# Kernel tuning notes

Hardware: AMD Instinct MI355X
Metric: run time of the kernel (lower is better)

The kernel has to match this reference:

```python
import jax, jax.numpy as jnp
import numpy as np

NUM_QRYS = 300
NUM_CLASSES = 80
NUM_PAIRS = 4_000_000
NMS_CANDIDATES = 1000
NMS_THR = 0.65
MAX_SEGS = 100
REFINED_WEIGHT = 2.0
FH = FW = 256  # final mask grid resolution


def setup_inputs() -> dict:
    key = jax.random.key(0)
    k1, k2, k3, k4, k5, k6, k7 = jax.random.split(key, 7)
    cls_logits = jax.random.normal(k1, (NUM_QRYS, NUM_CLASSES + 1), jnp.float32)
    # valid xyxy boxes in normalized [0,1] coords
    b = jax.random.uniform(k2, (NUM_QRYS, 4), jnp.float32)
    x1 = b[:, 0] * 0.7
    y1 = b[:, 1] * 0.7
    x2 = x1 + 0.05 + b[:, 2] * 0.25
    y2 = y1 + 0.05 + b[:, 3] * 0.25
    pred_boxes = jnp.stack([x1, y1, x2, y2], axis=1)
    seg_logits = jax.random.normal(k3, (NUM_PAIRS,), jnp.float32)
    key_xy = jax.random.uniform(k4, (NUM_PAIRS, 2), jnp.float32)
    qry_ids = jax.random.randint(k5, (NUM_PAIRS,), 0, NUM_QRYS, jnp.int32)
    refined_mask = jax.random.randint(k6, (NUM_PAIRS,), 0, 2, jnp.int32).astype(bool)
    map_ids = jax.random.randint(k7, (NUM_PAIRS,), 0, 4, jnp.int32)
    return {"cls_logits": cls_logits, "pred_boxes": pred_boxes, "seg_logits": seg_logits,
            "key_xy": key_xy, "qry_ids": qry_ids, "refined_mask": refined_mask, "map_ids": map_ids}


def _box_iou(boxes):  # boxes: [C,4] xyxy -> [C,C]
    x1 = jnp.maximum(boxes[:, None, 0], boxes[None, :, 0])
    y1 = jnp.maximum(boxes[:, None, 1], boxes[None, :, 1])
    x2 = jnp.minimum(boxes[:, None, 2], boxes[None, :, 2])
    y2 = jnp.minimum(boxes[:, None, 3], boxes[None, :, 3])
    inter = jnp.clip(x2 - x1, 0.0) * jnp.clip(y2 - y1, 0.0)
    area = (boxes[:, 2] - boxes[:, 0]) * (boxes[:, 3] - boxes[:, 1])
    union = area[:, None] + area[None, :] - inter
    return inter / jnp.maximum(union, 1e-9)


def _nms_keep(iou, thr):
    # greedy NMS over score-sorted candidates (rows already in descending score order)
    C = iou.shape[0]
    idx = jnp.arange(C)
    def body(i, keep):
        sup = (iou[i] > thr) & (idx > i) & keep[i]
        return keep & ~sup
    return jax.lax.fori_loop(0, C, body, jnp.ones(C, dtype=bool))


def reference(cls_logits, pred_boxes, seg_logits, key_xy, qry_ids, refined_mask, map_ids):
    num_qrys = cls_logits.shape[0]
    # expand per-query class scores -> flat predictions (batch_size = 1)
    scores = jax.nn.sigmoid(cls_logits[:, :-1]).reshape(-1)          # [Q*C]
    feat_ids = jnp.repeat(jnp.arange(num_qrys), NUM_CLASSES)          # [Q*C]
    labels = jnp.tile(jnp.arange(NUM_CLASSES), num_qrys)              # [Q*C]
    # top-k candidates before NMS
    top_scores, cand = jax.lax.top_k(scores, NMS_CANDIDATES)
    cand_feats = feat_ids[cand]
    cand_labels = labels[cand]
    # class-aware (batched) NMS: offset boxes per label so classes don't suppress each other
    offs = cand_labels.astype(pred_boxes.dtype)[:, None] * 4.0
    cand_boxes = pred_boxes[cand_feats] + offs
    keep = _nms_keep(_box_iou(cand_boxes), NMS_THR)
    kept_scores = jnp.where(keep, top_scores, -jnp.inf)
    sel_scores, sel = jax.lax.top_k(kept_scores, MAX_SEGS)
    sel_scores = jnp.where(jnp.isfinite(sel_scores), sel_scores, 0.0)
    sel_feats = cand_feats[sel]
    # assemble per-query mask logit maps from sparse query-key pairs (scatter-max)
    px = jnp.clip((key_xy[:, 0] * FW).astype(jnp.int32), 0, FW - 1)
    py = jnp.clip((key_xy[:, 1] * FH).astype(jnp.int32), 0, FH - 1)
    w_logits = jnp.where(refined_mask, REFINED_WEIGHT * seg_logits, seg_logits)
    flat = qry_ids * (FH * FW) + py * FW + px                          # [num_pairs]
    qry_maps = jnp.full((num_qrys * FH * FW,), -1e4, cls_logits.dtype).at[flat].max(w_logits)
    qry_maps = qry_maps.reshape(num_qrys, FH, FW)
    mask_probs = jax.nn.sigmoid(qry_maps[sel_feats])                   # [MAX_SEGS, FH, FW]
    # score-weighted soft masks (float output; thresholding at mask_thr yields bool masks)
    return sel_scores[:, None, None] * mask_probs
```

## Files before the change

kernel.cpp:

```cpp
#include <hip/hip_runtime.h>

#define NQ        300
#define NC        80
#define NE        24000
#define CAND      1000
#define KSEL      100
#define NPAIRS    4000000
#define HB        4096
#define FHW       65536
#define NMS_THR_F 0.65f
#define MAPS_INIT 0x39E3BFFFu

__device__ __forceinline__ unsigned enc_f32(float f) {
    unsigned u = __float_as_uint(f);
    return (u & 0x80000000u) ? ~u : (u | 0x80000000u);
}
__device__ __forceinline__ float dec_f32(unsigned k) {
    unsigned u = (k & 0x80000000u) ? (k ^ 0x80000000u) : ~k;
    return __uint_as_float(u);
}

__global__ void k_init_maps(uint4* __restrict__ maps) {
    int i = blockIdx.x * 256 + threadIdx.x;
    uint4 v; v.x = v.y = v.z = v.w = MAPS_INIT;
    maps[i] = v;
}

__global__ __launch_bounds__(1024) void k_select_sort(
    const float* __restrict__ cls,
    const float* __restrict__ pboxes,
    float4* __restrict__ cboxes, float* __restrict__ cscore,
    int* __restrict__ cfeat, int* __restrict__ clabel)
{
    __shared__ unsigned long long sbuf[4096];
    unsigned* hist = (unsigned*)sbuf;
    __shared__ unsigned subhist[64];
    __shared__ int sB, sT, sAbove, sCount, sN;
    int tid = threadIdx.x;

    for (int b = tid; b < HB; b += 1024) hist[b] = 0u;
    if (tid < 64) subhist[tid] = 0u;
    __syncthreads();

    unsigned long long lk[24];
    #pragma unroll
    for (int k = 0; k < 24; k++) {
        int e = tid + (k << 10);
        if (e < NE) {
            int q = e / NC, c = e - q * NC;
            float x = cls[q * (NC + 1) + c];
            float s = 1.f / (1.f + expf(-x));
            unsigned bits = __float_as_uint(s);
            lk[k] = ((unsigned long long)bits << 32) | (unsigned)(0xFFFFFFFFu - (unsigned)e);
            atomicAdd(&hist[bits >> 18], 1u);
        }
    }
    __syncthreads();

    if (tid == 0) {
        int acc = 0, B = 0;
        for (int b = HB - 1; b >= 0; b--) {
            acc += (int)hist[b];
            if (acc >= CAND) { B = b; break; }
        }
        sB = B; sAbove = acc - (int)hist[B]; sCount = 0;
    }
    __syncthreads();
    unsigned B = (unsigned)sB;

    #pragma unroll
    for (int k = 0; k < 24; k++) {
        int e = tid + (k << 10);
        if (e < NE && (unsigned)(lk[k] >> 50) == B)
            atomicAdd(&subhist[(unsigned)(lk[k] >> 44) & 63u], 1u);
    }
    __syncthreads();
    if (tid == 0) {
        int acc2 = sAbove, T = 0;
        for (int t = 63; t >= 0; t--) {
            acc2 += (int)subhist[t];
            if (acc2 >= CAND) { T = t; break; }
        }
        sT = T; sN = acc2;
    }
    __syncthreads();
    unsigned T = (unsigned)sT;

    #pragma unroll
    for (int k = 0; k < 24; k++) {
        int e = tid + (k << 10);
        if (e < NE) {
            unsigned long long key = lk[k];
            unsigned bkt = (unsigned)(key >> 50);
            unsigned sub = (unsigned)(key >> 44) & 63u;
            if (bkt > B || (bkt == B && sub >= T)) {
                int pos = atomicAdd(&sCount, 1);
                if (pos < 4096) sbuf[pos] = key;
            }
        }
    }
    __syncthreads();
    int n = min(sN, 4096);

    if (n <= 1024) {
        unsigned long long r = (tid < n) ? sbuf[tid] : 0ULL;
        for (int k = 2; k <= 1024; k <<= 1) {
            for (int j = k >> 1; j > 0; j >>= 1) {
                unsigned long long p;
                if (j >= 64) {
                    sbuf[tid] = r; __syncthreads();
                    p = sbuf[tid ^ j]; __syncthreads();
                } else {
                    p = __shfl_xor(r, j, 64);
                }
                bool d = (tid & k) != 0, lower = (tid & j) == 0;
                r = (d != lower) ? (r > p ? r : p) : (r < p ? r : p);
            }
        }
        sbuf[tid] = r;
        __syncthreads();
    } else {
        int nsort = 2048; while (nsort < n) nsort <<= 1;
        for (int i = n + tid; i < nsort; i += 1024) sbuf[i] = 0ULL;
        __syncthreads();
        for (int k = 2; k <= nsort; k <<= 1) {
            for (int j = k >> 1; j > 0; j >>= 1) {
                for (int i = tid; i < nsort; i += 1024) {
                    int ixj = i ^ j;
                    if (ixj > i) {
                        unsigned long long a = sbuf[i], b = sbuf[ixj];
                        bool up = ((i & k) == 0);
                        if (up ? (a < b) : (a > b)) { sbuf[i] = b; sbuf[ixj] = a; }
                    }
                }
                __syncthreads();
            }
        }
    }

    if (tid < CAND) {
        unsigned long long key = sbuf[tid];
        unsigned bits = (unsigned)(key >> 32);
        unsigned e = 0xFFFFFFFFu - (unsigned)(key & 0xFFFFFFFFu);
        int feat = (int)e / NC, lab = (int)e - feat * NC;
        cscore[tid] = __uint_as_float(bits);
        cfeat[tid]  = feat;
        clabel[tid] = lab;
        float off = 4.f * (float)lab;
        float4 b;
        b.x = pboxes[feat * 4 + 0] + off; b.y = pboxes[feat * 4 + 1] + off;
        b.z = pboxes[feat * 4 + 2] + off; b.w = pboxes[feat * 4 + 3] + off;
        cboxes[tid] = b;
    }
}

__global__ __launch_bounds__(64) void k_nms(
    const float4* __restrict__ cboxes, const int* __restrict__ clabel,
    int* __restrict__ keepflag)
{
    int lab = blockIdx.x, lane = threadIdx.x;
    __shared__ int list[256];
    int base = 0;
    for (int c = 0; c < CAND; c += 64) {
        int i = c + lane;
        bool m = (i < CAND) && (clabel[i] == lab);
        unsigned long long bal = __ballot(m);
        int rank = __popcll(bal & ((1ULL << lane) - 1ULL));
        if (m && base + rank < 256) list[base + rank] = i;
        base += __popcll(bal);
    }
    __syncthreads();
    int n = min(base, 256);

    float4 bx[4]; float area[4];
    unsigned keepm = 0;
    #pragma unroll
    for (int s = 0; s < 4; s++) {
        int j = (s << 6) + lane;
        if (j < n) {
            bx[s] = cboxes[list[j]];
            area[s] = (bx[s].z - bx[s].x) * (bx[s].w - bx[s].y);
            keepm |= (1u << s);
        }
    }
    #pragma unroll
    for (int slot = 0; slot < 4; slot++) {
        int i0 = slot << 6;
        if (i0 >= n) break;
        int iend = min(64, n - i0);
        for (int l = 0; l < iend; l++) {
            int i = i0 + l;
            unsigned km = __shfl(keepm, l);
            bool keep_i = (km >> slot) & 1u;
            float bix = __shfl(bx[slot].x, l), biy = __shfl(bx[slot].y, l);
            float biz = __shfl(bx[slot].z, l), biw = __shfl(bx[slot].w, l);
            float ai  = __shfl(area[slot], l);
            if (keep_i) {
                #pragma unroll
                for (int s2 = 0; s2 < 4; s2++) {
                    int j = (s2 << 6) + lane;
                    if (j > i && j < n && ((keepm >> s2) & 1u)) {
                        float xx1 = fmaxf(bix, bx[s2].x), yy1 = fmaxf(biy, bx[s2].y);
                        float xx2 = fminf(biz, bx[s2].z), yy2 = fminf(biw, bx[s2].w);
                        float inter = fmaxf(xx2 - xx1, 0.f) * fmaxf(yy2 - yy1, 0.f);
                        float uni = ai + area[s2] - inter;
                        if (inter / fmaxf(uni, 1e-9f) > NMS_THR_F) keepm &= ~(1u << s2);
                    }
                }
            }
        }
    }
    #pragma unroll
    for (int s = 0; s < 4; s++) {
        int j = (s << 6) + lane;
        if (j < n) keepflag[list[j]] = (keepm >> s) & 1u;
    }
}

__global__ __launch_bounds__(64) void k_pick(
    const float* __restrict__ cscore, const int* __restrict__ cfeat,
    const int* __restrict__ keepflag,
    float* __restrict__ sel_score, int* __restrict__ sel_slot,
    int* __restrict__ qry2slot,
    const unsigned* __restrict__ refined_raw, unsigned* __restrict__ mode_flag)
{
    int lane = threadIdx.x;
    __shared__ float ss[KSEL];
    __shared__ int   sf[KSEL];
    __shared__ int   q2s[NQ];

    unsigned any = 0;
    for (int i = lane; i < 4096; i += 64) if (refined_raw[i] > 1u) any = 1;
    unsigned mode = (__ballot(any != 0) != 0ULL) ? 1u : 0u;

    int base = 0;
    for (int c = 0; c < CAND; c += 64) {
        int i = c + lane;
        bool k = (i < CAND) && (keepflag[i] != 0);
        unsigned long long bal = __ballot(k);
        int rank = __popcll(bal & ((1ULL << lane) - 1ULL));
        int pos = base + rank;
        if (k && pos < KSEL) { ss[pos] = cscore[i]; sf[pos] = cfeat[i]; }
        base += __popcll(bal);
    }
    for (int q = lane; q < NQ; q += 64) q2s[q] = -1;
    __syncthreads();
    if (lane == 0) {
        int nsel = min(base, KSEL), nslots = 0;
        for (int s = 0; s < KSEL; s++) {
            if (s < nsel) {
                int f = sf[s];
                int sl = q2s[f];
                if (sl < 0) { sl = nslots++; q2s[f] = sl; }
                sel_slot[s] = sl; sel_score[s] = ss[s];
            } else {
                sel_slot[s] = -1; sel_score[s] = 0.f;
            }
        }
        *mode_flag = mode;
    }
    __syncthreads();
    for (int q = lane; q < NQ; q += 64) qry2slot[q] = q2s[q];
}

__global__ __launch_bounds__(256) void k_scatter(
    const float* __restrict__ seg, const float2* __restrict__ xy,
    const int* __restrict__ qry, const unsigned* __restrict__ refined_raw,
    const int* __restrict__ qry2slot, const unsigned* __restrict__ mode_flag,
    unsigned* __restrict__ maps)
{
    int t = blockIdx.x * 256 + threadIdx.x;
    int base = t << 2;
    if (base >= NPAIRS) return;

    int4 q4 = ((const int4*)qry)[t];
    int s0 = qry2slot[q4.x], s1 = qry2slot[q4.y];
    int s2 = qry2slot[q4.z], s3 = qry2slot[q4.w];
    if ((s0 & s1 & s2 & s3) < 0) return;

    float4 sg   = ((const float4*)seg)[t];
    float4 xy01 = ((const float4*)xy)[2 * t];
    float4 xy23 = ((const float4*)xy)[2 * t + 1];
    unsigned r0, r1, r2, r3;
    if (*mode_flag) {
        unsigned rb = refined_raw[t];
        r0 = rb & 255u; r1 = (rb >> 8) & 255u; r2 = (rb >> 16) & 255u; r3 = rb >> 24;
    } else {
        uint4 rr = ((const uint4*)refined_raw)[t];
        r0 = rr.x; r1 = rr.y; r2 = rr.z; r3 = rr.w;
    }

    #define DO_PAIR(S, PX, PY, W, R)                                              \
        if (S >= 0) {                                                             \
            int px = min(max((int)((PX) * 256.f), 0), 255);                       \
            int py = min(max((int)((PY) * 256.f), 0), 255);                       \
            float w = (R) ? 2.f * (W) : (W);                                      \
            atomicMax(&maps[S * FHW + py * 256 + px], enc_f32(w));                \
        }
    DO_PAIR(s0, xy01.x, xy01.y, sg.x, r0)
    DO_PAIR(s1, xy01.z, xy01.w, sg.y, r1)
    DO_PAIR(s2, xy23.x, xy23.y, sg.z, r2)
    DO_PAIR(s3, xy23.z, xy23.w, sg.w, r3)
    #undef DO_PAIR
}

__global__ __launch_bounds__(256) void k_output(
    const uint4* __restrict__ maps4,
    const float* __restrict__ sel_score, const int* __restrict__ sel_slot,
    float4* __restrict__ out4)
{
    int i = blockIdx.x * 256 + threadIdx.x;
    int s = i >> 14;
    float sc = sel_score[s];
    int slot = sel_slot[s];
    float4 v = {0.f, 0.f, 0.f, 0.f};
    if (slot >= 0) {
        uint4 m = maps4[slot * (FHW / 4) + (i & 16383)];
        v.x = sc / (1.f + expf(-dec_f32(m.x)));
        v.y = sc / (1.f + expf(-dec_f32(m.y)));
        v.z = sc / (1.f + expf(-dec_f32(m.z)));
        v.w = sc / (1.f + expf(-dec_f32(m.w)));
    }
    out4[i] = v;
}

extern "C" void kernel_launch(void* const* d_in, const int* in_sizes, int n_in,
                              void* d_out, int out_size, void* d_ws, size_t ws_size,
                              hipStream_t stream) {
    const float*    cls     = (const float*)d_in[0];
    const float*    pboxes  = (const float*)d_in[1];
    const float*    seg     = (const float*)d_in[2];
    const float2*   xy      = (const float2*)d_in[3];
    const int*      qry     = (const int*)d_in[4];
    const unsigned* refined = (const unsigned*)d_in[5];
    float* out = (float*)d_out;

    char* ws = (char*)d_ws;
    unsigned*  maps      = (unsigned*)ws;
    float4*    cboxes    = (float4*)(ws + 26214400);
    float*     cscore    = (float*) (ws + 26230400);
    int*       cfeat     = (int*)   (ws + 26234400);
    int*       clabel    = (int*)   (ws + 26238400);
    int*       keepflag  = (int*)   (ws + 26242400);
    float*     sel_score = (float*) (ws + 26246400);
    int*       sel_slot  = (int*)   (ws + 26246800);
    int*       qry2slot  = (int*)   (ws + 26247200);
    unsigned*  mode_flag = (unsigned*)(ws + 26248400);

    k_init_maps  <<<6400, 256, 0, stream>>>((uint4*)maps);
    k_select_sort<<<1, 1024, 0, stream>>>(cls, pboxes, cboxes, cscore, cfeat, clabel);
    k_nms        <<<NC, 64, 0, stream>>>(cboxes, clabel, keepflag);
    k_pick       <<<1, 64, 0, stream>>>(cscore, cfeat, keepflag, sel_score, sel_slot,
                                        qry2slot, refined, mode_flag);
    k_scatter    <<<3907, 256, 0, stream>>>(seg, xy, qry, refined, qry2slot, mode_flag, maps);
    k_output     <<<6400, 256, 0, stream>>>((const uint4*)maps, sel_score, sel_slot,
                                            (float4*)out);
}
```

Baseline: 256.0 us.

## Fuse map init into select, merge NMS and pick, widen scatter to 8 pairs

Map initialization now runs in extra blocks of the top-k selection kernel. Per-class NMS and final selection are merged into one 1024-thread block, with 16 waves each taking classes in turn and keep flags held in shared memory. The scatter kernel now handles 8 pairs per thread and stages the query-to-slot table in shared memory, issuing all loads before the barrier. Together these cut two launches and their inter-kernel gaps, at the cost of running NMS on a single workgroup instead of 80.

```diff
diff --git a/kernel.cpp b/kernel.cpp
--- a/kernel.cpp
+++ b/kernel.cpp
@@ -20,23 +20,25 @@
     return __uint_as_float(u);
 }
 
-__global__ void k_init_maps(uint4* __restrict__ maps) {
-    int i = blockIdx.x * 256 + threadIdx.x;
-    uint4 v; v.x = v.y = v.z = v.w = MAPS_INIT;
-    maps[i] = v;
-}
-
-__global__ __launch_bounds__(1024) void k_select_sort(
+__global__ __launch_bounds__(1024) void k_init_select(
     const float* __restrict__ cls,
     const float* __restrict__ pboxes,
     float4* __restrict__ cboxes, float* __restrict__ cscore,
-    int* __restrict__ cfeat, int* __restrict__ clabel)
+    int* __restrict__ cfeat, int* __restrict__ clabel,
+    uint4* __restrict__ maps)
 {
     __shared__ unsigned long long sbuf[4096];
     unsigned* hist = (unsigned*)sbuf;
     __shared__ unsigned subhist[64];
     __shared__ int sB, sT, sAbove, sCount, sN;
     int tid = threadIdx.x;
+
+    if (blockIdx.x != 0) {
+        int i = (blockIdx.x - 1) * 1024 + tid;
+        uint4 v; v.x = v.y = v.z = v.w = MAPS_INIT;
+        maps[i] = v;
+        return;
+    }
 
     for (int b = tid; b < HB; b += 1024) hist[b] = 0u;
     if (tid < 64) subhist[tid] = 0u;
@@ -154,99 +156,109 @@
     }
 }
 
-__global__ __launch_bounds__(64) void k_nms(
+__global__ __launch_bounds__(1024) void k_nms_pick(
     const float4* __restrict__ cboxes, const int* __restrict__ clabel,
-    int* __restrict__ keepflag)
-{
-    int lab = blockIdx.x, lane = threadIdx.x;
-    __shared__ int list[256];
-    int base = 0;
-    for (int c = 0; c < CAND; c += 64) {
-        int i = c + lane;
-        bool m = (i < CAND) && (clabel[i] == lab);
-        unsigned long long bal = __ballot(m);
-        int rank = __popcll(bal & ((1ULL << lane) - 1ULL));
-        if (m && base + rank < 256) list[base + rank] = i;
-        base += __popcll(bal);
-    }
-    __syncthreads();
-    int n = min(base, 256);
-
-    float4 bx[4]; float area[4];
-    unsigned keepm = 0;
-    #pragma unroll
-    for (int s = 0; s < 4; s++) {
-        int j = (s << 6) + lane;
-        if (j < n) {
-            bx[s] = cboxes[list[j]];
-            area[s] = (bx[s].z - bx[s].x) * (bx[s].w - bx[s].y);
-            keepm |= (1u << s);
-        }
-    }
-    #pragma unroll
-    for (int slot = 0; slot < 4; slot++) {
-        int i0 = slot << 6;
-        if (i0 >= n) break;
-        int iend = min(64, n - i0);
-        for (int l = 0; l < iend; l++) {
-            int i = i0 + l;
-            unsigned km = __shfl(keepm, l);
-            bool keep_i = (km >> slot) & 1u;
-            float bix = __shfl(bx[slot].x, l), biy = __shfl(bx[slot].y, l);
-            float biz = __shfl(bx[slot].z, l), biw = __shfl(bx[slot].w, l);
-            float ai  = __shfl(area[slot], l);
-            if (keep_i) {
-                #pragma unroll
-                for (int s2 = 0; s2 < 4; s2++) {
-                    int j = (s2 << 6) + lane;
-                    if (j > i && j < n && ((keepm >> s2) & 1u)) {
-                        float xx1 = fmaxf(bix, bx[s2].x), yy1 = fmaxf(biy, bx[s2].y);
-                        float xx2 = fminf(biz, bx[s2].z), yy2 = fminf(biw, bx[s2].w);
-                        float inter = fmaxf(xx2 - xx1, 0.f) * fmaxf(yy2 - yy1, 0.f);
-                        float uni = ai + area[s2] - inter;
-                        if (inter / fmaxf(uni, 1e-9f) > NMS_THR_F) keepm &= ~(1u << s2);
-                    }
-                }
-            }
-        }
-    }
-    #pragma unroll
-    for (int s = 0; s < 4; s++) {
-        int j = (s << 6) + lane;
-        if (j < n) keepflag[list[j]] = (keepm >> s) & 1u;
-    }
-}
-
-__global__ __launch_bounds__(64) void k_pick(
     const float* __restrict__ cscore, const int* __restrict__ cfeat,
-    const int* __restrict__ keepflag,
     float* __restrict__ sel_score, int* __restrict__ sel_slot,
     int* __restrict__ qry2slot,
     const unsigned* __restrict__ refined_raw, unsigned* __restrict__ mode_flag)
 {
-    int lane = threadIdx.x;
+    __shared__ int list[16][256];
+    __shared__ int keepf[CAND];
     __shared__ float ss[KSEL];
     __shared__ int   sf[KSEL];
     __shared__ int   q2s[NQ];
-
-    unsigned any = 0;
-    for (int i = lane; i < 4096; i += 64) if (refined_raw[i] > 1u) any = 1;
-    unsigned mode = (__ballot(any != 0) != 0ULL) ? 1u : 0u;
-
-    int base = 0;
-    for (int c = 0; c < CAND; c += 64) {
-        int i = c + lane;
-        bool k = (i < CAND) && (keepflag[i] != 0);
-        unsigned long long bal = __ballot(k);
-        int rank = __popcll(bal & ((1ULL << lane) - 1ULL));
-        int pos = base + rank;
-        if (k && pos < KSEL) { ss[pos] = cscore[i]; sf[pos] = cfeat[i]; }
-        base += __popcll(bal);
-    }
-    for (int q = lane; q < NQ; q += 64) q2s[q] = -1;
-    __syncthreads();
-    if (lane == 0) {
-        int nsel = min(base, KSEL), nslots = 0;
+    __shared__ unsigned smode;
+    __shared__ int sbase;
+
+    int tid  = threadIdx.x;
+    int wave = tid >> 6, lane = tid & 63;
+    int* mylist = list[wave];
+
+    for (int i = tid; i < CAND; i += 1024) keepf[i] = 0;
+    for (int q = tid; q < NQ; q += 1024) q2s[q] = -1;
+    __syncthreads();
+
+    for (int lab = wave; lab < NC; lab += 16) {
+        int base = 0;
+        for (int c = 0; c < CAND; c += 64) {
+            int i = c + lane;
+            bool m = (i < CAND) && (clabel[i] == lab);
+            unsigned long long bal = __ballot(m);
+            int rank = __popcll(bal & ((1ULL << lane) - 1ULL));
+            if (m && base + rank < 256) mylist[base + rank] = i;
+            base += __popcll(bal);
+        }
+        int n = min(base, 256);
+
+        float4 bx[4]; float area[4];
+        unsigned keepm = 0;
+        #pragma unroll
+        for (int s = 0; s < 4; s++) {
+            int j = (s << 6) + lane;
+            if (j < n) {
+                bx[s] = cboxes[mylist[j]];
+                area[s] = (bx[s].z - bx[s].x) * (bx[s].w - bx[s].y);
+                keepm |= (1u << s);
+            }
+        }
+        #pragma unroll
+        for (int slot = 0; slot < 4; slot++) {
+            int i0 = slot << 6;
+            if (i0 >= n) break;
+            int iend = min(64, n - i0);
+            for (int l = 0; l < iend; l++) {
+                int i = i0 + l;
+                unsigned km = __shfl(keepm, l);
+                bool keep_i = (km >> slot) & 1u;
+                float bix = __shfl(bx[slot].x, l), biy = __shfl(bx[slot].y, l);
+                float biz = __shfl(bx[slot].z, l), biw = __shfl(bx[slot].w, l);
+                float ai  = __shfl(area[slot], l);
+                if (keep_i) {
+                    #pragma unroll
+                    for (int s2 = 0; s2 < 4; s2++) {
+                        int j = (s2 << 6) + lane;
+                        if (j > i && j < n && ((keepm >> s2) & 1u)) {
+                            float xx1 = fmaxf(bix, bx[s2].x), yy1 = fmaxf(biy, bx[s2].y);
+                            float xx2 = fminf(biz, bx[s2].z), yy2 = fminf(biw, bx[s2].w);
+                            float inter = fmaxf(xx2 - xx1, 0.f) * fmaxf(yy2 - yy1, 0.f);
+                            float uni = ai + area[s2] - inter;
+                            if (inter / fmaxf(uni, 1e-9f) > NMS_THR_F) keepm &= ~(1u << s2);
+                        }
+                    }
+                }
+            }
+        }
+        #pragma unroll
+        for (int s = 0; s < 4; s++) {
+            int j = (s << 6) + lane;
+            if (j < n) keepf[mylist[j]] = (keepm >> s) & 1u;
+        }
+    }
+    __syncthreads();
+
+    if (wave == 0) {
+        unsigned any = 0;
+        for (int i = lane; i < 4096; i += 64) if (refined_raw[i] > 1u) any = 1;
+        unsigned mode = (__ballot(any != 0) != 0ULL) ? 1u : 0u;
+        if (lane == 0) smode = mode;
+
+        int base = 0;
+        for (int c = 0; c < CAND; c += 64) {
+            int i = c + lane;
+            bool k = (i < CAND) && (keepf[i] != 0);
+            unsigned long long bal = __ballot(k);
+            int rank = __popcll(bal & ((1ULL << lane) - 1ULL));
+            int pos = base + rank;
+            if (k && pos < KSEL) { ss[pos] = cscore[i]; sf[pos] = cfeat[i]; }
+            base += __popcll(bal);
+        }
+        if (lane == 0) sbase = base;
+    }
+    __syncthreads();
+
+    if (tid == 0) {
+        int nsel = min(sbase, KSEL), nslots = 0;
         for (int s = 0; s < KSEL; s++) {
             if (s < nsel) {
                 int f = sf[s];
@@ -257,38 +269,53 @@
                 sel_slot[s] = -1; sel_score[s] = 0.f;
             }
         }
-        *mode_flag = mode;
-    }
-    __syncthreads();
-    for (int q = lane; q < NQ; q += 64) qry2slot[q] = q2s[q];
+        *mode_flag = smode;
+    }
+    __syncthreads();
+    for (int q = tid; q < NQ; q += 1024) qry2slot[q] = q2s[q];
 }
 
 __global__ __launch_bounds__(256) void k_scatter(
-    const float* __restrict__ seg, const float2* __restrict__ xy,
-    const int* __restrict__ qry, const unsigned* __restrict__ refined_raw,
+    const float4* __restrict__ seg4, const float4* __restrict__ xy4,
+    const int4* __restrict__ qry4, const unsigned* __restrict__ refined_raw,
     const int* __restrict__ qry2slot, const unsigned* __restrict__ mode_flag,
     unsigned* __restrict__ maps)
 {
-    int t = blockIdx.x * 256 + threadIdx.x;
-    int base = t << 2;
-    if (base >= NPAIRS) return;
-
-    int4 q4 = ((const int4*)qry)[t];
-    int s0 = qry2slot[q4.x], s1 = qry2slot[q4.y];
-    int s2 = qry2slot[q4.z], s3 = qry2slot[q4.w];
-    if ((s0 & s1 & s2 & s3) < 0) return;
-
-    float4 sg   = ((const float4*)seg)[t];
-    float4 xy01 = ((const float4*)xy)[2 * t];
-    float4 xy23 = ((const float4*)xy)[2 * t + 1];
-    unsigned r0, r1, r2, r3;
-    if (*mode_flag) {
-        unsigned rb = refined_raw[t];
-        r0 = rb & 255u; r1 = (rb >> 8) & 255u; r2 = (rb >> 16) & 255u; r3 = rb >> 24;
-    } else {
-        uint4 rr = ((const uint4*)refined_raw)[t];
-        r0 = rr.x; r1 = rr.y; r2 = rr.z; r3 = rr.w;
-    }
+    __shared__ int q2s[NQ];
+    int tid = threadIdx.x;
+    int t = blockIdx.x * 256 + tid;
+    bool act = (t < (NPAIRS / 8));
+
+    int4 qa = {0,0,0,0}, qb = {0,0,0,0};
+    float4 sa = {0,0,0,0}, sb = {0,0,0,0};
+    float4 x0 = {0,0,0,0}, x1 = {0,0,0,0}, x2 = {0,0,0,0}, x3 = {0,0,0,0};
+    unsigned r0=0,r1=0,r2=0,r3=0,r4=0,r5=0,r6=0,r7=0;
+
+    if (act) {
+        qa = qry4[2*t];     qb = qry4[2*t+1];
+        sa = seg4[2*t];     sb = seg4[2*t+1];
+        x0 = xy4[4*t];      x1 = xy4[4*t+1];
+        x2 = xy4[4*t+2];    x3 = xy4[4*t+3];
+        unsigned mode = *mode_flag;
+        if (mode) {
+            unsigned rw0 = refined_raw[2*t], rw1 = refined_raw[2*t+1];
+            r0 = rw0 & 255u; r1 = (rw0 >> 8) & 255u; r2 = (rw0 >> 16) & 255u; r3 = rw0 >> 24;
+            r4 = rw1 & 255u; r5 = (rw1 >> 8) & 255u; r6 = (rw1 >> 16) & 255u; r7 = rw1 >> 24;
+        } else {
+            uint4 rr0 = ((const uint4*)refined_raw)[2*t];
+            uint4 rr1 = ((const uint4*)refined_raw)[2*t+1];
+            r0 = rr0.x; r1 = rr0.y; r2 = rr0.z; r3 = rr0.w;
+            r4 = rr1.x; r5 = rr1.y; r6 = rr1.z; r7 = rr1.w;
+        }
+    }
+
+    for (int q = tid; q < NQ; q += 256) q2s[q] = qry2slot[q];
+    __syncthreads();
+    if (!act) return;
+
+    int s0 = q2s[qa.x], s1 = q2s[qa.y], s2 = q2s[qa.z], s3 = q2s[qa.w];
+    int s4 = q2s[qb.x], s5 = q2s[qb.y], s6 = q2s[qb.z], s7 = q2s[qb.w];
+    if ((s0 & s1 & s2 & s3 & s4 & s5 & s6 & s7) < 0) return;
 
     #define DO_PAIR(S, PX, PY, W, R)                                              \
         if (S >= 0) {                                                             \
@@ -297,10 +324,14 @@
             float w = (R) ? 2.f * (W) : (W);                                      \
             atomicMax(&maps[S * FHW + py * 256 + px], enc_f32(w));                \
         }
-    DO_PAIR(s0, xy01.x, xy01.y, sg.x, r0)
-    DO_PAIR(s1, xy01.z, xy01.w, sg.y, r1)
-    DO_PAIR(s2, xy23.x, xy23.y, sg.z, r2)
-    DO_PAIR(s3, xy23.z, xy23.w, sg.w, r3)
+    DO_PAIR(s0, x0.x, x0.y, sa.x, r0)
+    DO_PAIR(s1, x0.z, x0.w, sa.y, r1)
+    DO_PAIR(s2, x1.x, x1.y, sa.z, r2)
+    DO_PAIR(s3, x1.z, x1.w, sa.w, r3)
+    DO_PAIR(s4, x2.x, x2.y, sb.x, r4)
+    DO_PAIR(s5, x2.z, x2.w, sb.y, r5)
+    DO_PAIR(s6, x3.x, x3.y, sb.z, r6)
+    DO_PAIR(s7, x3.z, x3.w, sb.w, r7)
     #undef DO_PAIR
 }
 
@@ -329,9 +360,9 @@
                               hipStream_t stream) {
     const float*    cls     = (const float*)d_in[0];
     const float*    pboxes  = (const float*)d_in[1];
-    const float*    seg     = (const float*)d_in[2];
-    const float2*   xy      = (const float2*)d_in[3];
-    const int*      qry     = (const int*)d_in[4];
+    const float4*   seg4    = (const float4*)d_in[2];
+    const float4*   xy4     = (const float4*)d_in[3];
+    const int4*     qry4    = (const int4*)d_in[4];
     const unsigned* refined = (const unsigned*)d_in[5];
     float* out = (float*)d_out;
 
@@ -341,18 +372,17 @@
     float*     cscore    = (float*) (ws + 26230400);
     int*       cfeat     = (int*)   (ws + 26234400);
     int*       clabel    = (int*)   (ws + 26238400);
-    int*       keepflag  = (int*)   (ws + 26242400);
     float*     sel_score = (float*) (ws + 26246400);
     int*       sel_slot  = (int*)   (ws + 26246800);
     int*       qry2slot  = (int*)   (ws + 26247200);
     unsigned*  mode_flag = (unsigned*)(ws + 26248400);
 
-    k_init_maps  <<<6400, 256, 0, stream>>>((uint4*)maps);
-    k_select_sort<<<1, 1024, 0, stream>>>(cls, pboxes, cboxes, cscore, cfeat, clabel);
-    k_nms        <<<NC, 64, 0, stream>>>(cboxes, clabel, keepflag);
-    k_pick       <<<1, 64, 0, stream>>>(cscore, cfeat, keepflag, sel_score, sel_slot,
-                                        qry2slot, refined, mode_flag);
-    k_scatter    <<<3907, 256, 0, stream>>>(seg, xy, qry, refined, qry2slot, mode_flag, maps);
+    k_init_select<<<1601, 1024, 0, stream>>>(cls, pboxes, cboxes, cscore, cfeat, clabel,
+                                             (uint4*)maps);
+    k_nms_pick   <<<1, 1024, 0, stream>>>(cboxes, clabel, cscore, cfeat,
+                                          sel_score, sel_slot, qry2slot, refined, mode_flag);
+    k_scatter    <<<1954, 256, 0, stream>>>(seg4, xy4, qry4, refined, qry2slot, mode_flag,
+                                            (unsigned*)maps);
     k_output     <<<6400, 256, 0, stream>>>((const uint4*)maps, sel_score, sel_slot,
                                             (float4*)out);
 }
```

New measurement: 260.7 us. About the same (+1.8%).

## Bin selected pairs per slot, then build mask tiles in shared memory

Applied to the files above, without the earlier changes.

Replaces the global atomicMax scatter into a 26 MB per-slot map, and the kernel that initialised it, with a two-phase scheme. A staging kernel buckets the selected pairs into per-slot bins using block-local histograms and one global tail counter per slot. A tile kernel then rebuilds each 8192-pixel tile with shared-memory atomicMax and writes the sigmoid-weighted output directly. This removes the map initialisation pass and the global-memory atomics. The cost is that each tile block rescans the whole bin of its slot, so every bin is read eight times. A fixed per-slot capacity of 32768 records silently drops overflow pairs when a query has more pairs than that.

```diff
diff --git a/kernel.cpp b/kernel.cpp
--- a/kernel.cpp
+++ b/kernel.cpp
@@ -11,6 +11,9 @@
 #define NMS_THR_F 0.65f
 #define MAPS_INIT 0x39E3BFFFu
 
+#define NBLK_A    977
+#define SLOT_CAP  32768
+
 __device__ __forceinline__ unsigned enc_f32(float f) {
     unsigned u = __float_as_uint(f);
     return (u & 0x80000000u) ? ~u : (u | 0x80000000u);
@@ -20,23 +23,20 @@
     return __uint_as_float(u);
 }
 
-__global__ void k_init_maps(uint4* __restrict__ maps) {
-    int i = blockIdx.x * 256 + threadIdx.x;
-    uint4 v; v.x = v.y = v.z = v.w = MAPS_INIT;
-    maps[i] = v;
-}
-
-__global__ __launch_bounds__(1024) void k_select_sort(
+__global__ __launch_bounds__(1024) void k_select(
     const float* __restrict__ cls,
     const float* __restrict__ pboxes,
     float4* __restrict__ cboxes, float* __restrict__ cscore,
-    int* __restrict__ cfeat, int* __restrict__ clabel)
+    int* __restrict__ cfeat, int* __restrict__ clabel,
+    unsigned* __restrict__ slot_tail)
 {
     __shared__ unsigned long long sbuf[4096];
     unsigned* hist = (unsigned*)sbuf;
     __shared__ unsigned subhist[64];
     __shared__ int sB, sT, sAbove, sCount, sN;
     int tid = threadIdx.x;
+
+    if (tid < KSEL) slot_tail[tid] = 0u;
 
     for (int b = tid; b < HB; b += 1024) hist[b] = 0u;
     if (tid < 64) subhist[tid] = 0u;
@@ -263,65 +263,112 @@
     for (int q = lane; q < NQ; q += 64) qry2slot[q] = q2s[q];
 }
 
-__global__ __launch_bounds__(256) void k_scatter(
-    const float* __restrict__ seg, const float2* __restrict__ xy,
-    const int* __restrict__ qry, const unsigned* __restrict__ refined_raw,
+__global__ __launch_bounds__(1024) void k_stage(
+    const float4* __restrict__ seg4, const float4* __restrict__ xy4,
+    const int4* __restrict__ qry4, const unsigned* __restrict__ refined_raw,
     const int* __restrict__ qry2slot, const unsigned* __restrict__ mode_flag,
-    unsigned* __restrict__ maps)
+    unsigned long long* __restrict__ bins, unsigned* __restrict__ slot_tail)
 {
-    int t = blockIdx.x * 256 + threadIdx.x;
-    int base = t << 2;
-    if (base >= NPAIRS) return;
-
-    int4 q4 = ((const int4*)qry)[t];
-    int s0 = qry2slot[q4.x], s1 = qry2slot[q4.y];
-    int s2 = qry2slot[q4.z], s3 = qry2slot[q4.w];
-    if ((s0 & s1 & s2 & s3) < 0) return;
-
-    float4 sg   = ((const float4*)seg)[t];
-    float4 xy01 = ((const float4*)xy)[2 * t];
-    float4 xy23 = ((const float4*)xy)[2 * t + 1];
-    unsigned r0, r1, r2, r3;
-    if (*mode_flag) {
-        unsigned rb = refined_raw[t];
-        r0 = rb & 255u; r1 = (rb >> 8) & 255u; r2 = (rb >> 16) & 255u; r3 = rb >> 24;
-    } else {
-        uint4 rr = ((const uint4*)refined_raw)[t];
-        r0 = rr.x; r1 = rr.y; r2 = rr.z; r3 = rr.w;
-    }
-
-    #define DO_PAIR(S, PX, PY, W, R)                                              \
-        if (S >= 0) {                                                             \
-            int px = min(max((int)((PX) * 256.f), 0), 255);                       \
-            int py = min(max((int)((PY) * 256.f), 0), 255);                       \
-            float w = (R) ? 2.f * (W) : (W);                                      \
-            atomicMax(&maps[S * FHW + py * 256 + px], enc_f32(w));                \
-        }
-    DO_PAIR(s0, xy01.x, xy01.y, sg.x, r0)
-    DO_PAIR(s1, xy01.z, xy01.w, sg.y, r1)
-    DO_PAIR(s2, xy23.x, xy23.y, sg.z, r2)
-    DO_PAIR(s3, xy23.z, xy23.w, sg.w, r3)
-    #undef DO_PAIR
-}
-
-__global__ __launch_bounds__(256) void k_output(
-    const uint4* __restrict__ maps4,
+    __shared__ unsigned hist[KSEL];
+    __shared__ unsigned gbase[KSEL];
+    int tid = threadIdx.x, b = blockIdx.x;
+    if (tid < KSEL) hist[tid] = 0u;
+    __syncthreads();
+
+    int t = b * 1024 + tid;
+    unsigned addr[4], encw[4], rnk[4]; int nloc = 0;
+    if (t < (NPAIRS / 4)) {
+        int4 q = qry4[t];
+        int s0 = qry2slot[q.x], s1 = qry2slot[q.y];
+        int s2 = qry2slot[q.z], s3 = qry2slot[q.w];
+        if ((s0 & s1 & s2 & s3) >= 0 || s0 >= 0 || s1 >= 0 || s2 >= 0 || s3 >= 0) {
+            float4 sg   = seg4[t];
+            float4 xy01 = xy4[2 * t], xy23 = xy4[2 * t + 1];
+            unsigned r0, r1, r2, r3;
+            if (*mode_flag) {
+                unsigned rb = refined_raw[t];
+                r0 = rb & 255u; r1 = (rb >> 8) & 255u; r2 = (rb >> 16) & 255u; r3 = rb >> 24;
+            } else {
+                uint4 rr = ((const uint4*)refined_raw)[t];
+                r0 = rr.x; r1 = rr.y; r2 = rr.z; r3 = rr.w;
+            }
+            #define MK_REC(S, PX, PY, W, R)                                       \
+                if (S >= 0) {                                                     \
+                    int px = min(max((int)((PX) * 256.f), 0), 255);               \
+                    int py = min(max((int)((PY) * 256.f), 0), 255);               \
+                    float w = (R) ? 2.f * (W) : (W);                              \
+                    addr[nloc] = ((unsigned)S << 16) | ((unsigned)py << 8) | (unsigned)px; \
+                    encw[nloc] = enc_f32(w);                                      \
+                    rnk[nloc]  = atomicAdd(&hist[S], 1u);                         \
+                    nloc++;                                                       \
+                }
+            MK_REC(s0, xy01.x, xy01.y, sg.x, r0)
+            MK_REC(s1, xy01.z, xy01.w, sg.y, r1)
+            MK_REC(s2, xy23.x, xy23.y, sg.z, r2)
+            MK_REC(s3, xy23.z, xy23.w, sg.w, r3)
+            #undef MK_REC
+        }
+    }
+    __syncthreads();
+    if (tid < KSEL && hist[tid] > 0u)
+        gbase[tid] = atomicAdd(&slot_tail[tid], hist[tid]);
+    __syncthreads();
+
+    for (int k = 0; k < nloc; k++) {
+        unsigned s = addr[k] >> 16;
+        unsigned pos = gbase[s] + rnk[k];
+        if (pos < SLOT_CAP)
+            bins[(size_t)s * SLOT_CAP + pos] =
+                ((unsigned long long)encw[k] << 32) | addr[k];
+    }
+}
+
+__global__ __launch_bounds__(1024) void k_tile_out(
+    const unsigned long long* __restrict__ bins,
+    const unsigned* __restrict__ slot_tail,
     const float* __restrict__ sel_score, const int* __restrict__ sel_slot,
     float4* __restrict__ out4)
 {
-    int i = blockIdx.x * 256 + threadIdx.x;
-    int s = i >> 14;
-    float sc = sel_score[s];
-    int slot = sel_slot[s];
-    float4 v = {0.f, 0.f, 0.f, 0.f};
-    if (slot >= 0) {
-        uint4 m = maps4[slot * (FHW / 4) + (i & 16383)];
-        v.x = sc / (1.f + expf(-dec_f32(m.x)));
-        v.y = sc / (1.f + expf(-dec_f32(m.y)));
-        v.z = sc / (1.f + expf(-dec_f32(m.z)));
-        v.w = sc / (1.f + expf(-dec_f32(m.w)));
-    }
-    out4[i] = v;
+    __shared__ unsigned tile[8192];
+    int tid = threadIdx.x;
+    int i = blockIdx.x >> 3, h = blockIdx.x & 7;
+    int slot = sel_slot[i];
+    float sc = sel_score[i];
+    long obase = (long)i * (FHW / 4) + h * 2048;
+
+    if (slot < 0) {
+        float4 z = {0.f, 0.f, 0.f, 0.f};
+        out4[obase + tid] = z;
+        out4[obase + 1024 + tid] = z;
+        return;
+    }
+
+    #pragma unroll
+    for (int k = 0; k < 8; k++) tile[tid + (k << 10)] = MAPS_INIT;
+    __syncthreads();
+
+    unsigned tot = min(slot_tail[slot], (unsigned)SLOT_CAP);
+    const unsigned long long* seg = bins + (size_t)slot * SLOT_CAP;
+    for (unsigned j = tid; j < tot; j += 1024) {
+        unsigned long long r = seg[j];
+        unsigned addr = (unsigned)r;
+        if (((addr >> 13) & 7u) == (unsigned)h)
+            atomicMax(&tile[addr & 8191u], (unsigned)(r >> 32));
+    }
+    __syncthreads();
+
+    #pragma unroll
+    for (int k = 0; k < 2; k++) {
+        int j = tid + (k << 10);
+        unsigned m0 = tile[4 * j + 0], m1 = tile[4 * j + 1];
+        unsigned m2 = tile[4 * j + 2], m3 = tile[4 * j + 3];
+        float4 v;
+        v.x = sc / (1.f + expf(-dec_f32(m0)));
+        v.y = sc / (1.f + expf(-dec_f32(m1)));
+        v.z = sc / (1.f + expf(-dec_f32(m2)));
+        v.w = sc / (1.f + expf(-dec_f32(m3)));
+        out4[obase + j] = v;
+    }
 }
 
 extern "C" void kernel_launch(void* const* d_in, const int* in_sizes, int n_in,
@@ -329,30 +376,32 @@
                               hipStream_t stream) {
     const float*    cls     = (const float*)d_in[0];
     const float*    pboxes  = (const float*)d_in[1];
-    const float*    seg     = (const float*)d_in[2];
-    const float2*   xy      = (const float2*)d_in[3];
-    const int*      qry     = (const int*)d_in[4];
+    const float4*   seg4    = (const float4*)d_in[2];
+    const float4*   xy4     = (const float4*)d_in[3];
+    const int4*     qry4    = (const int4*)d_in[4];
     const unsigned* refined = (const unsigned*)d_in[5];
     float* out = (float*)d_out;
 
     char* ws = (char*)d_ws;
-    unsigned*  maps      = (unsigned*)ws;
-    float4*    cboxes    = (float4*)(ws + 26214400);
-    float*     cscore    = (float*) (ws + 26230400);
-    int*       cfeat     = (int*)   (ws + 26234400);
-    int*       clabel    = (int*)   (ws + 26238400);
-    int*       keepflag  = (int*)   (ws + 26242400);
-    float*     sel_score = (float*) (ws + 26246400);
-    int*       sel_slot  = (int*)   (ws + 26246800);
-    int*       qry2slot  = (int*)   (ws + 26247200);
-    unsigned*  mode_flag = (unsigned*)(ws + 26248400);
-
-    k_init_maps  <<<6400, 256, 0, stream>>>((uint4*)maps);
-    k_select_sort<<<1, 1024, 0, stream>>>(cls, pboxes, cboxes, cscore, cfeat, clabel);
-    k_nms        <<<NC, 64, 0, stream>>>(cboxes, clabel, keepflag);
-    k_pick       <<<1, 64, 0, stream>>>(cscore, cfeat, keepflag, sel_score, sel_slot,
-                                        qry2slot, refined, mode_flag);
-    k_scatter    <<<3907, 256, 0, stream>>>(seg, xy, qry, refined, qry2slot, mode_flag, maps);
-    k_output     <<<6400, 256, 0, stream>>>((const uint4*)maps, sel_score, sel_slot,
-                                            (float4*)out);
-}
+    unsigned long long* bins = (unsigned long long*)ws;
+    unsigned*  slot_tail = (unsigned*)(ws + 26214400);
+    float4*    cboxes    = (float4*)  (ws + 26214800);
+    float*     cscore    = (float*)   (ws + 26230800);
+    int*       cfeat     = (int*)     (ws + 26234800);
+    int*       clabel    = (int*)     (ws + 26238800);
+    int*       keepflag  = (int*)     (ws + 26242800);
+    float*     sel_score = (float*)   (ws + 26246800);
+    int*       sel_slot  = (int*)     (ws + 26247200);
+    int*       qry2slot  = (int*)     (ws + 26247600);
+    unsigned*  mode_flag = (unsigned*)(ws + 26248800);
+
+    k_select  <<<1, 1024, 0, stream>>>(cls, pboxes, cboxes, cscore, cfeat, clabel,
+                                       slot_tail);
+    k_nms     <<<NC, 64, 0, stream>>>(cboxes, clabel, keepflag);
+    k_pick    <<<1, 64, 0, stream>>>(cscore, cfeat, keepflag, sel_score, sel_slot,
+                                     qry2slot, refined, mode_flag);
+    k_stage   <<<NBLK_A, 1024, 0, stream>>>(seg4, xy4, qry4, refined, qry2slot, mode_flag,
+                                            bins, slot_tail);
+    k_tile_out<<<KSEL * 8, 1024, 0, stream>>>(bins, slot_tail, sel_score, sel_slot,
+                                              (float4*)out);
+}
```

Measured after the change: 242.5 us. 1.06x faster.
